# Kernel optimization log

Hardware: AMD Instinct MI355X
Metric: run time of the kernel (lower is better)

Reference implementation:

```python
import jax, jax.numpy as jnp
import numpy as np

B, T, I, H, FUT = 16384, 50, 6, 128, 30


def setup_inputs() -> dict:
    key = jax.random.key(0)
    ks = jax.random.split(key, 10)
    bound = 1.0 / np.sqrt(H)
    u = lambda k, shape: jax.random.uniform(k, shape, jnp.float32, -bound, bound)
    return {
        "history": jax.random.normal(ks[0], (B, T, I), jnp.float32),
        # GRU weights (PyTorch layout: gates stacked [r, z, n])
        "w_ih": u(ks[1], (3 * H, I)),
        "w_hh": u(ks[2], (3 * H, H)),
        "b_ih": u(ks[3], (3 * H,)),
        "b_hh": u(ks[4], (3 * H,)),
        # MLP head: Linear(H,H) -> ReLU -> Linear(H,I)
        "w1": u(ks[5], (H, H)),
        "b1": u(ks[6], (H,)),
        "w2": u(ks[7], (I, H)),
        "b2": u(ks[8], (I,)),
    }


def _gru_cell(h, x, w_ih, w_hh, b_ih, b_hh):
    # PyTorch GRU cell: gates ordered r, z, n
    gi = x @ w_ih.T + b_ih          # (B, 3H)
    gh = h @ w_hh.T + b_hh          # (B, 3H)
    i_r, i_z, i_n = jnp.split(gi, 3, axis=-1)
    h_r, h_z, h_n = jnp.split(gh, 3, axis=-1)
    r = jax.nn.sigmoid(i_r + h_r)
    z = jax.nn.sigmoid(i_z + h_z)
    n = jnp.tanh(i_n + r * h_n)
    return (1.0 - z) * n + z * h


def reference(history, w_ih, w_hh, b_ih, b_hh, w1, b1, w2, b2):
    # --- encode history: scan GRU over time ---
    h0 = jnp.zeros((history.shape[0], H), history.dtype)

    def enc_step(h, x_t):
        return _gru_cell(h, x_t, w_ih, w_hh, b_ih, b_hh), None

    h_last, _ = jax.lax.scan(enc_step, h0, jnp.swapaxes(history, 0, 1))  # (B, H)

    def head(h):
        return jax.nn.relu(h @ w1.T + b1) @ w2.T + b2  # (B, I)

    def dec_step(carry, _):
        h, x = carry
        h = _gru_cell(h, x, w_ih, w_hh, b_ih, b_hh)
        x = head(h)
        return (h, x), x

    x0 = history[:, -1]  # (B, I)
    _, preds = jax.lax.scan(dec_step, (h_last, x0), None, length=FUT)  # (FUT, B, I)
    return jnp.swapaxes(preds, 0, 1)  # (B, FUT, I)
```

## Files before the change

kernel.cpp:

```cpp
#include <hip/hip_runtime.h>

typedef _Float16 half8 __attribute__((ext_vector_type(8)));
typedef float f32x4 __attribute__((ext_vector_type(4)));

#define ROWS 32
#define HA_PITCH 168
#define A1_PITCH 136
#define HBUF (ROWS * HA_PITCH)
#define LOG2E 1.442695041f

#define MFMA(a, b, c) __builtin_amdgcn_mfma_f32_16x16x32_f16((a), (b), (c), 0, 0, 0)

__global__ __launch_bounds__(256, 2)
void traj_gru(const float* __restrict__ history,
              const float* __restrict__ w_ih, const float* __restrict__ w_hh,
              const float* __restrict__ b_ih, const float* __restrict__ b_hh,
              const float* __restrict__ w1, const float* __restrict__ b1,
              const float* __restrict__ w2, const float* __restrict__ b2,
              float* __restrict__ out)
{
    __shared__ __align__(16) _Float16 hbuf[2 * HBUF];
    __shared__ __align__(16) _Float16 a1s[ROWS * A1_PITCH];

    const int tid  = threadIdx.x;
    const int wave = tid >> 6;
    const int lane = tid & 63;
    const int ln16 = lane & 15;
    const int q    = lane >> 4;
    const int rowbase = blockIdx.x * ROWS;
    const int cbase = wave * 32;

    for (int idx = tid; idx < 2 * HBUF; idx += 256) {
        int col = idx % HA_PITCH;
        hbuf[idx] = (col == 134) ? (_Float16)1.0f : (_Float16)0.0f;
    }

    half8 Bh[3][2][4];
    #pragma unroll
    for (int g = 0; g < 3; ++g) {
        float sc = (g < 2) ? -LOG2E : -2.0f * LOG2E;
        #pragma unroll
        for (int s = 0; s < 2; ++s)
            #pragma unroll
            for (int kt = 0; kt < 4; ++kt) {
                int n = g * 128 + cbase + s * 16 + ln16;
                const float* p = w_hh + n * 128 + kt * 32 + q * 8;
                half8 v;
                #pragma unroll
                for (int j = 0; j < 8; ++j) v[j] = (_Float16)(p[j] * sc);
                Bh[g][s][kt] = v;
            }
    }

    half8 Bi[3][2];
    #pragma unroll
    for (int g = 0; g < 3; ++g) {
        float sc = (g < 2) ? -LOG2E : -2.0f * LOG2E;
        #pragma unroll
        for (int s = 0; s < 2; ++s) {
            int n = g * 128 + cbase + s * 16 + ln16;
            half8 v;
            #pragma unroll
            for (int j = 0; j < 8; ++j) v[j] = (_Float16)0.0f;
            if (q == 0) {
                #pragma unroll
                for (int j = 0; j < 6; ++j) v[j] = (_Float16)(w_ih[n * 6 + j] * sc);
                float bias = b_ih[n] + (g < 2 ? b_hh[n] : 0.0f);
                v[6] = (_Float16)(bias * sc);
            }
            Bi[g][s] = v;
        }
    }

    float bhn[2], b1r[2];
    #pragma unroll
    for (int s = 0; s < 2; ++s) {
        bhn[s] = b_hh[256 + cbase + s * 16 + ln16] * (-2.0f * LOG2E);
        b1r[s] = b1[cbase + s * 16 + ln16];
    }

    half8 Bw1[2][4];
    #pragma unroll
    for (int s = 0; s < 2; ++s)
        #pragma unroll
        for (int kt = 0; kt < 4; ++kt) {
            int n = cbase + s * 16 + ln16;
            const float* p = w1 + n * 128 + kt * 32 + q * 8;
            half8 v;
            #pragma unroll
            for (int j = 0; j < 8; ++j) v[j] = (_Float16)p[j];
            Bw1[s][kt] = v;
        }

    half8 Bw2[4];
    #pragma unroll
    for (int kt = 0; kt < 4; ++kt) {
        half8 v;
        #pragma unroll
        for (int j = 0; j < 8; ++j) v[j] = (_Float16)0.0f;
        if (ln16 < 6) {
            const float* p = w2 + ln16 * 128 + kt * 32 + q * 8;
            #pragma unroll
            for (int j = 0; j < 8; ++j) v[j] = (_Float16)p[j];
        }
        Bw2[kt] = v;
    }
    float b2r = (ln16 < 6) ? b2[ln16] : 0.0f;

    float hp[2][2][4] = {};

    const int  xr = tid / 6;
    const int  xc = tid - xr * 6;
    const bool xactive = tid < ROWS * 6;

    __syncthreads();

    if (xactive)
        hbuf[xr * HA_PITCH + 128 + xc] = (_Float16)history[(rowbase + xr) * 300 + xc];
    __syncthreads();

    auto gru_step = [&](int p, int next_t) {
        const _Float16* hb = hbuf + p * HBUF;
        _Float16*       hn = hbuf + (p ^ 1) * HBUF;
        #pragma unroll
        for (int mt = 0; mt < 2; ++mt) {
            half8 Ah[4], Ax;
            const _Float16* rp = hb + (mt * 16 + ln16) * HA_PITCH;
            #pragma unroll
            for (int kt = 0; kt < 4; ++kt)
                Ah[kt] = *(const half8*)(rp + kt * 32 + q * 8);
            Ax = *(const half8*)(rp + 128 + q * 8);
            #pragma unroll
            for (int s = 0; s < 2; ++s) {
                f32x4 ar = {0,0,0,0}, az = {0,0,0,0}, ah = {0,0,0,0}, an = {0,0,0,0};
                #pragma unroll
                for (int kt = 0; kt < 4; ++kt) {
                    ar = MFMA(Ah[kt], Bh[0][s][kt], ar);
                    az = MFMA(Ah[kt], Bh[1][s][kt], az);
                    ah = MFMA(Ah[kt], Bh[2][s][kt], ah);
                }
                ar = MFMA(Ax, Bi[0][s], ar);
                az = MFMA(Ax, Bi[1][s], az);
                an = MFMA(Ax, Bi[2][s], an);
                #pragma unroll
                for (int i = 0; i < 4; ++i) {
                    float r = __builtin_amdgcn_rcpf(1.0f + __builtin_amdgcn_exp2f(ar[i]));
                    float z = __builtin_amdgcn_rcpf(1.0f + __builtin_amdgcn_exp2f(az[i]));
                    float t = an[i] + r * (ah[i] + bhn[s]);
                    float n = 2.0f * __builtin_amdgcn_rcpf(1.0f + __builtin_amdgcn_exp2f(t)) - 1.0f;
                    float h = n + z * (hp[mt][s][i] - n);
                    hp[mt][s][i] = h;
                    hn[(mt * 16 + q * 4 + i) * HA_PITCH + cbase + s * 16 + ln16] = (_Float16)h;
                }
            }
        }
        if (next_t >= 0 && xactive)
            hn[xr * HA_PITCH + 128 + xc] =
                (_Float16)history[(rowbase + xr) * 300 + next_t * 6 + xc];
        __syncthreads();
    };

    auto head_step = [&](int f, int p) {
        const _Float16* hb = hbuf + p * HBUF;
        _Float16*       hx = hbuf + p * HBUF;
        #pragma unroll
        for (int mt = 0; mt < 2; ++mt) {
            half8 Ahh[4];
            const _Float16* rp = hb + (mt * 16 + ln16) * HA_PITCH;
            #pragma unroll
            for (int kt = 0; kt < 4; ++kt)
                Ahh[kt] = *(const half8*)(rp + kt * 32 + q * 8);
            #pragma unroll
            for (int s = 0; s < 2; ++s) {
                f32x4 a = {0,0,0,0};
                #pragma unroll
                for (int kt = 0; kt < 4; ++kt)
                    a = MFMA(Ahh[kt], Bw1[s][kt], a);
                #pragma unroll
                for (int i = 0; i < 4; ++i) {
                    float v = a[i] + b1r[s];
                    v = v > 0.0f ? v : 0.0f;
                    a1s[(mt * 16 + q * 4 + i) * A1_PITCH + cbase + s * 16 + ln16] = (_Float16)v;
                }
            }
        }
        __syncthreads();
        if (wave < 2) {
            f32x4 o = {0,0,0,0};
            #pragma unroll
            for (int kt = 0; kt < 4; ++kt) {
                half8 Aa = *(const half8*)&a1s[(wave * 16 + ln16) * A1_PITCH + kt * 32 + q * 8];
                o = MFMA(Aa, Bw2[kt], o);
            }
            if (ln16 < 6) {
                #pragma unroll
                for (int i = 0; i < 4; ++i) {
                    int row = wave * 16 + q * 4 + i;
                    float v = o[i] + b2r;
                    out[(rowbase + row) * 180 + f * 6 + ln16] = v;
                    hx[row * HA_PITCH + 128 + ln16] = (_Float16)v;
                }
            }
        }
        __syncthreads();
    };

    int p = 0;
    #pragma unroll 1
    for (int t = 0; t < 50; ++t) {
        gru_step(p, t < 49 ? t + 1 : 49);
        p ^= 1;
    }
    #pragma unroll 1
    for (int f = 0; f < 30; ++f) {
        gru_step(p, -1);
        p ^= 1;
        head_step(f, p);
    }
}

extern "C" void kernel_launch(void* const* d_in, const int* in_sizes, int n_in,
                              void* d_out, int out_size, void* d_ws, size_t ws_size,
                              hipStream_t stream) {
    (void)in_sizes; (void)n_in; (void)d_ws; (void)ws_size; (void)out_size;
    traj_gru<<<dim3(16384 / ROWS), dim3(256), 0, stream>>>(
        (const float*)d_in[0], (const float*)d_in[1], (const float*)d_in[2],
        (const float*)d_in[3], (const float*)d_in[4], (const float*)d_in[5],
        (const float*)d_in[6], (const float*)d_in[7], (const float*)d_in[8],
        (float*)d_out);
}
```

Baseline: 295.3 us.

## Split GRU columns across 8 waves and preload history into LDS

Doubles the block to 512 threads, so each wave owns 16 hidden columns instead of 32, halving per-wave MFMA work and weight registers per step. The whole 50-step history slice is loaded once into LDS with a bias-one column, which takes the per-step global history load off the serial recurrence. W2 is staged in LDS instead of registers, and A-operand loads are software-pipelined across k-tiles. The cost is more waves contending at each barrier, a larger LDS footprint that can limit how many blocks fit per CU, and redundant loads of h by more waves.

```diff
diff --git a/kernel.cpp b/kernel.cpp
--- a/kernel.cpp
+++ b/kernel.cpp
@@ -4,14 +4,12 @@
 typedef float f32x4 __attribute__((ext_vector_type(4)));
 
 #define ROWS 32
-#define HA_PITCH 168
-#define A1_PITCH 136
-#define HBUF (ROWS * HA_PITCH)
+#define HP 136
+#define HBUFSZ (ROWS * HP)
 #define LOG2E 1.442695041f
-
 #define MFMA(a, b, c) __builtin_amdgcn_mfma_f32_16x16x32_f16((a), (b), (c), 0, 0, 0)
 
-__global__ __launch_bounds__(256, 2)
+__global__ __launch_bounds__(512, 4)
 void traj_gru(const float* __restrict__ history,
               const float* __restrict__ w_ih, const float* __restrict__ w_hh,
               const float* __restrict__ b_ih, const float* __restrict__ b_hh,
@@ -19,8 +17,11 @@
               const float* __restrict__ w2, const float* __restrict__ b2,
               float* __restrict__ out)
 {
-    __shared__ __align__(16) _Float16 hbuf[2 * HBUF];
-    __shared__ __align__(16) _Float16 a1s[ROWS * A1_PITCH];
+    __shared__ __align__(16) _Float16 hbuf[2 * HBUFSZ];
+    __shared__ __align__(16) _Float16 xhist[50 * ROWS * 8];
+    __shared__ __align__(16) _Float16 xdec[ROWS * 8];
+    __shared__ __align__(16) _Float16 a1s[ROWS * HP];
+    __shared__ __align__(16) _Float16 w2f[4 * 4 * 16 * 8];
 
     const int tid  = threadIdx.x;
     const int wave = tid >> 6;
@@ -28,160 +29,133 @@
     const int ln16 = lane & 15;
     const int q    = lane >> 4;
     const int rowbase = blockIdx.x * ROWS;
-    const int cbase = wave * 32;
-
-    for (int idx = tid; idx < 2 * HBUF; idx += 256) {
-        int col = idx % HA_PITCH;
-        hbuf[idx] = (col == 134) ? (_Float16)1.0f : (_Float16)0.0f;
-    }
-
-    half8 Bh[3][2][4];
+    const int cbase = wave * 16;
+
+    for (int i = tid; i < 2 * HBUFSZ; i += 512) hbuf[i] = (_Float16)0;
+    for (int i = tid; i < 50 * ROWS * 8; i += 512) xhist[i] = (_Float16)0;
+    for (int i = tid; i < ROWS * 8; i += 512) xdec[i] = (_Float16)0;
+    for (int i = tid; i < 4 * 4 * 16 * 8; i += 512) w2f[i] = (_Float16)0;
+    __syncthreads();
+
+    for (int idx = tid; idx < ROWS * 300; idx += 512) {
+        int r = idx / 300, rem = idx - r * 300;
+        int t = rem / 6, c = rem - t * 6;
+        xhist[(t * ROWS + r) * 8 + c] = (_Float16)history[(rowbase + r) * 300 + rem];
+    }
+    for (int idx = tid; idx < 50 * ROWS; idx += 512)
+        xhist[idx * 8 + 6] = (_Float16)1.0f;
+    for (int idx = tid; idx < ROWS; idx += 512)
+        xdec[idx * 8 + 6] = (_Float16)1.0f;
+    for (int idx = tid; idx < 6 * 128; idx += 512) {
+        int n = idx >> 7, k = idx & 127;
+        int kt = k >> 5, qq = (k >> 3) & 3, j = k & 7;
+        w2f[((kt * 4 + qq) * 16 + n) * 8 + j] = (_Float16)w2[n * 128 + k];
+    }
+
+    half8 Bh[3][4];
     #pragma unroll
     for (int g = 0; g < 3; ++g) {
         float sc = (g < 2) ? -LOG2E : -2.0f * LOG2E;
         #pragma unroll
-        for (int s = 0; s < 2; ++s)
-            #pragma unroll
-            for (int kt = 0; kt < 4; ++kt) {
-                int n = g * 128 + cbase + s * 16 + ln16;
-                const float* p = w_hh + n * 128 + kt * 32 + q * 8;
-                half8 v;
-                #pragma unroll
-                for (int j = 0; j < 8; ++j) v[j] = (_Float16)(p[j] * sc);
-                Bh[g][s][kt] = v;
-            }
-    }
-
-    half8 Bi[3][2];
+        for (int kt = 0; kt < 4; ++kt) {
+            int n = g * 128 + cbase + ln16;
+            const float* p = w_hh + n * 128 + kt * 32 + q * 8;
+            half8 v;
+            #pragma unroll
+            for (int j = 0; j < 8; ++j) v[j] = (_Float16)(p[j] * sc);
+            Bh[g][kt] = v;
+        }
+    }
+    half8 Bi[3];
     #pragma unroll
     for (int g = 0; g < 3; ++g) {
         float sc = (g < 2) ? -LOG2E : -2.0f * LOG2E;
-        #pragma unroll
-        for (int s = 0; s < 2; ++s) {
-            int n = g * 128 + cbase + s * 16 + ln16;
-            half8 v;
-            #pragma unroll
-            for (int j = 0; j < 8; ++j) v[j] = (_Float16)0.0f;
-            if (q == 0) {
-                #pragma unroll
-                for (int j = 0; j < 6; ++j) v[j] = (_Float16)(w_ih[n * 6 + j] * sc);
-                float bias = b_ih[n] + (g < 2 ? b_hh[n] : 0.0f);
-                v[6] = (_Float16)(bias * sc);
-            }
-            Bi[g][s] = v;
-        }
-    }
-
-    float bhn[2], b1r[2];
-    #pragma unroll
-    for (int s = 0; s < 2; ++s) {
-        bhn[s] = b_hh[256 + cbase + s * 16 + ln16] * (-2.0f * LOG2E);
-        b1r[s] = b1[cbase + s * 16 + ln16];
-    }
-
-    half8 Bw1[2][4];
-    #pragma unroll
-    for (int s = 0; s < 2; ++s)
-        #pragma unroll
-        for (int kt = 0; kt < 4; ++kt) {
-            int n = cbase + s * 16 + ln16;
-            const float* p = w1 + n * 128 + kt * 32 + q * 8;
-            half8 v;
-            #pragma unroll
-            for (int j = 0; j < 8; ++j) v[j] = (_Float16)p[j];
-            Bw1[s][kt] = v;
-        }
-
-    half8 Bw2[4];
+        int n = g * 128 + cbase + ln16;
+        half8 v;
+        #pragma unroll
+        for (int j = 0; j < 8; ++j) v[j] = (_Float16)0.0f;
+        if (q == 0) {
+            #pragma unroll
+            for (int j = 0; j < 6; ++j) v[j] = (_Float16)(w_ih[n * 6 + j] * sc);
+            v[6] = (_Float16)((b_ih[n] + (g < 2 ? b_hh[n] : 0.0f)) * sc);
+        }
+        Bi[g] = v;
+    }
+    const float bhn = b_hh[256 + cbase + ln16] * (-2.0f * LOG2E);
+    half8 Bw1[4];
     #pragma unroll
     for (int kt = 0; kt < 4; ++kt) {
+        int n = cbase + ln16;
+        const float* p = w1 + n * 128 + kt * 32 + q * 8;
         half8 v;
         #pragma unroll
-        for (int j = 0; j < 8; ++j) v[j] = (_Float16)0.0f;
-        if (ln16 < 6) {
-            const float* p = w2 + ln16 * 128 + kt * 32 + q * 8;
-            #pragma unroll
-            for (int j = 0; j < 8; ++j) v[j] = (_Float16)p[j];
-        }
-        Bw2[kt] = v;
-    }
-    float b2r = (ln16 < 6) ? b2[ln16] : 0.0f;
-
-    float hp[2][2][4] = {};
-
-    const int  xr = tid / 6;
-    const int  xc = tid - xr * 6;
-    const bool xactive = tid < ROWS * 6;
+        for (int j = 0; j < 8; ++j) v[j] = (_Float16)p[j];
+        Bw1[kt] = v;
+    }
+    const float b1r = b1[cbase + ln16];
+    const float b2r = (ln16 < 6) ? b2[ln16] : 0.0f;
+
+    float hp[2][4] = {};
 
     __syncthreads();
 
-    if (xactive)
-        hbuf[xr * HA_PITCH + 128 + xc] = (_Float16)history[(rowbase + xr) * 300 + xc];
-    __syncthreads();
-
-    auto gru_step = [&](int p, int next_t) {
-        const _Float16* hb = hbuf + p * HBUF;
-        _Float16*       hn = hbuf + (p ^ 1) * HBUF;
+    auto gru_step = [&](int p, const _Float16* xp) {
+        const _Float16* hb = hbuf + p * HBUFSZ;
+        _Float16*       hn = hbuf + (p ^ 1) * HBUFSZ;
         #pragma unroll
         for (int mt = 0; mt < 2; ++mt) {
-            half8 Ah[4], Ax;
-            const _Float16* rp = hb + (mt * 16 + ln16) * HA_PITCH;
-            #pragma unroll
-            for (int kt = 0; kt < 4; ++kt)
-                Ah[kt] = *(const half8*)(rp + kt * 32 + q * 8);
-            Ax = *(const half8*)(rp + 128 + q * 8);
-            #pragma unroll
-            for (int s = 0; s < 2; ++s) {
-                f32x4 ar = {0,0,0,0}, az = {0,0,0,0}, ah = {0,0,0,0}, an = {0,0,0,0};
-                #pragma unroll
-                for (int kt = 0; kt < 4; ++kt) {
-                    ar = MFMA(Ah[kt], Bh[0][s][kt], ar);
-                    az = MFMA(Ah[kt], Bh[1][s][kt], az);
-                    ah = MFMA(Ah[kt], Bh[2][s][kt], ah);
-                }
-                ar = MFMA(Ax, Bi[0][s], ar);
-                az = MFMA(Ax, Bi[1][s], az);
-                an = MFMA(Ax, Bi[2][s], an);
-                #pragma unroll
-                for (int i = 0; i < 4; ++i) {
-                    float r = __builtin_amdgcn_rcpf(1.0f + __builtin_amdgcn_exp2f(ar[i]));
-                    float z = __builtin_amdgcn_rcpf(1.0f + __builtin_amdgcn_exp2f(az[i]));
-                    float t = an[i] + r * (ah[i] + bhn[s]);
-                    float n = 2.0f * __builtin_amdgcn_rcpf(1.0f + __builtin_amdgcn_exp2f(t)) - 1.0f;
-                    float h = n + z * (hp[mt][s][i] - n);
-                    hp[mt][s][i] = h;
-                    hn[(mt * 16 + q * 4 + i) * HA_PITCH + cbase + s * 16 + ln16] = (_Float16)h;
-                }
-            }
-        }
-        if (next_t >= 0 && xactive)
-            hn[xr * HA_PITCH + 128 + xc] =
-                (_Float16)history[(rowbase + xr) * 300 + next_t * 6 + xc];
+            const _Float16* rp = hb + (mt * 16 + ln16) * HP + q * 8;
+            half8 Ax = {0,0,0,0,0,0,0,0};
+            if (q == 0) Ax = *(const half8*)(xp + (mt * 16 + ln16) * 8);
+            f32x4 ar = {0,0,0,0}, az = {0,0,0,0}, ah = {0,0,0,0}, an = {0,0,0,0};
+            half8 Acur = *(const half8*)(rp);
+            #pragma unroll
+            for (int kt = 0; kt < 4; ++kt) {
+                half8 Anext;
+                if (kt < 3) Anext = *(const half8*)(rp + (kt + 1) * 32);
+                ar = MFMA(Acur, Bh[0][kt], ar);
+                az = MFMA(Acur, Bh[1][kt], az);
+                ah = MFMA(Acur, Bh[2][kt], ah);
+                Acur = Anext;
+            }
+            ar = MFMA(Ax, Bi[0], ar);
+            az = MFMA(Ax, Bi[1], az);
+            an = MFMA(Ax, Bi[2], an);
+            _Float16* wp = hn + (mt * 16 + q * 4) * HP + cbase + ln16;
+            #pragma unroll
+            for (int i = 0; i < 4; ++i) {
+                float r = __builtin_amdgcn_rcpf(1.0f + __builtin_amdgcn_exp2f(ar[i]));
+                float z = __builtin_amdgcn_rcpf(1.0f + __builtin_amdgcn_exp2f(az[i]));
+                float t = an[i] + r * (ah[i] + bhn);
+                float n = 2.0f * __builtin_amdgcn_rcpf(1.0f + __builtin_amdgcn_exp2f(t)) - 1.0f;
+                float h = n + z * (hp[mt][i] - n);
+                hp[mt][i] = h;
+                wp[i * HP] = (_Float16)h;
+            }
+        }
         __syncthreads();
     };
 
     auto head_step = [&](int f, int p) {
-        const _Float16* hb = hbuf + p * HBUF;
-        _Float16*       hx = hbuf + p * HBUF;
+        const _Float16* hb = hbuf + p * HBUFSZ;
         #pragma unroll
         for (int mt = 0; mt < 2; ++mt) {
-            half8 Ahh[4];
-            const _Float16* rp = hb + (mt * 16 + ln16) * HA_PITCH;
-            #pragma unroll
-            for (int kt = 0; kt < 4; ++kt)
-                Ahh[kt] = *(const half8*)(rp + kt * 32 + q * 8);
-            #pragma unroll
-            for (int s = 0; s < 2; ++s) {
-                f32x4 a = {0,0,0,0};
-                #pragma unroll
-                for (int kt = 0; kt < 4; ++kt)
-                    a = MFMA(Ahh[kt], Bw1[s][kt], a);
-                #pragma unroll
-                for (int i = 0; i < 4; ++i) {
-                    float v = a[i] + b1r[s];
-                    v = v > 0.0f ? v : 0.0f;
-                    a1s[(mt * 16 + q * 4 + i) * A1_PITCH + cbase + s * 16 + ln16] = (_Float16)v;
-                }
+            const _Float16* rp = hb + (mt * 16 + ln16) * HP + q * 8;
+            f32x4 a = {0,0,0,0};
+            half8 Acur = *(const half8*)(rp);
+            #pragma unroll
+            for (int kt = 0; kt < 4; ++kt) {
+                half8 Anext;
+                if (kt < 3) Anext = *(const half8*)(rp + (kt + 1) * 32);
+                a = MFMA(Acur, Bw1[kt], a);
+                Acur = Anext;
+            }
+            _Float16* wp = a1s + (mt * 16 + q * 4) * HP + cbase + ln16;
+            #pragma unroll
+            for (int i = 0; i < 4; ++i) {
+                float v = a[i] + b1r;
+                v = v > 0.0f ? v : 0.0f;
+                wp[i * HP] = (_Float16)v;
             }
         }
         __syncthreads();
@@ -189,8 +163,9 @@
             f32x4 o = {0,0,0,0};
             #pragma unroll
             for (int kt = 0; kt < 4; ++kt) {
-                half8 Aa = *(const half8*)&a1s[(wave * 16 + ln16) * A1_PITCH + kt * 32 + q * 8];
-                o = MFMA(Aa, Bw2[kt], o);
+                half8 Aa = *(const half8*)&a1s[(wave * 16 + ln16) * HP + kt * 32 + q * 8];
+                half8 Bw = *(const half8*)&w2f[((kt * 4 + q) * 16 + ln16) * 8];
+                o = MFMA(Aa, Bw, o);
             }
             if (ln16 < 6) {
                 #pragma unroll
@@ -198,7 +173,7 @@
                     int row = wave * 16 + q * 4 + i;
                     float v = o[i] + b2r;
                     out[(rowbase + row) * 180 + f * 6 + ln16] = v;
-                    hx[row * HA_PITCH + 128 + ln16] = (_Float16)v;
+                    xdec[row * 8 + ln16] = (_Float16)v;
                 }
             }
         }
@@ -207,13 +182,10 @@
 
     int p = 0;
     #pragma unroll 1
-    for (int t = 0; t < 50; ++t) {
-        gru_step(p, t < 49 ? t + 1 : 49);
-        p ^= 1;
-    }
+    for (int t = 0; t < 50; ++t) { gru_step(p, xhist + t * ROWS * 8); p ^= 1; }
     #pragma unroll 1
     for (int f = 0; f < 30; ++f) {
-        gru_step(p, -1);
+        gru_step(p, f == 0 ? xhist + 49 * ROWS * 8 : xdec);
         p ^= 1;
         head_step(f, p);
     }
@@ -223,7 +195,7 @@
                               void* d_out, int out_size, void* d_ws, size_t ws_size,
                               hipStream_t stream) {
     (void)in_sizes; (void)n_in; (void)d_ws; (void)ws_size; (void)out_size;
-    traj_gru<<<dim3(16384 / ROWS), dim3(256), 0, stream>>>(
+    traj_gru<<<dim3(16384 / ROWS), dim3(512), 0, stream>>>(
         (const float*)d_in[0], (const float*)d_in[1], (const float*)d_in[2],
         (const float*)d_in[3], (const float*)d_in[4], (const float*)d_in[5],
         (const float*)d_in[6], (const float*)d_in[7], (const float*)d_in[8],
```

Result: faster. 287.4 us (-2.7%).
